# Kernel tuning notes

Hardware: AMD Instinct MI355X
Metric: run time of the kernel (lower is better)

Reference implementation:

```python
import jax, jax.numpy as jnp
import numpy as np

B, S, D, H = 4, 2048, 1024, 16
DEPTH = D // H


def setup_inputs() -> dict:
    key = jax.random.key(0)
    ks = jax.random.split(key, 12)
    q = jax.random.normal(ks[0], (B, S, D), dtype=jnp.float32)
    k = jax.random.normal(ks[1], (B, S, D), dtype=jnp.float32)
    v = jax.random.normal(ks[2], (B, S, D), dtype=jnp.float32)
    # causal mask: 1.0 where attention is disallowed (upper triangle), per `mask * -1e9`
    mask = 1.0 - jnp.tril(jnp.ones((S, S), dtype=jnp.float32))
    mask = mask[None, None, :, :]  # [1,1,S,S] broadcastable over batch/heads
    scale = 1.0 / np.sqrt(D)
    Wq = jax.random.normal(ks[3], (D, D), dtype=jnp.float32) * scale
    Wk = jax.random.normal(ks[4], (D, D), dtype=jnp.float32) * scale
    Wv = jax.random.normal(ks[5], (D, D), dtype=jnp.float32) * scale
    Wo = jax.random.normal(ks[6], (D, D), dtype=jnp.float32) * scale
    bq = jnp.zeros((D,), jnp.float32)
    bk = jnp.zeros((D,), jnp.float32)
    bv = jnp.zeros((D,), jnp.float32)
    bo = jnp.zeros((D,), jnp.float32)
    return {"query": q, "key": k, "value": v, "mask": mask,
            "Wq": Wq, "bq": bq, "Wk": Wk, "bk": bk,
            "Wv": Wv, "bv": bv, "Wo": Wo, "bo": bo}


def _split_heads(x):
    # [B, S, D] -> [B, H, S, depth]
    b, s, _ = x.shape
    return x.reshape(b, s, H, DEPTH).transpose(0, 2, 1, 3)


def reference(query, key, value, mask, Wq, bq, Wk, bk, Wv, bv, Wo, bo):
    q = _split_heads(query @ Wq + bq)   # [B,H,S,depth]
    k = _split_heads(key @ Wk + bk)
    v = _split_heads(value @ Wv + bv)
    scores = jnp.einsum('bhqd,bhkd->bhqk', q, k) / jnp.sqrt(
        jnp.asarray(DEPTH, q.dtype))
    scores = scores + mask * (-1e9)
    attn = jax.nn.softmax(scores, axis=-1)
    out = jnp.einsum('bhqk,bhkd->bhqd', attn, v)   # [B,H,S,depth]
    out = out.transpose(0, 2, 1, 3).reshape(query.shape[0], -1, H * DEPTH)
    return out @ Wo + bo
```

## Files before the change

kernel.cpp:

```cpp
#include <hip/hip_runtime.h>

#define Bsz 4
#define SEQ 2048
#define DIM 1024
#define NH 16
#define HD 64

typedef float  f32x4  __attribute__((ext_vector_type(4)));
typedef __bf16 bf16x8 __attribute__((ext_vector_type(8)));
typedef __bf16 bf16x4 __attribute__((ext_vector_type(4)));
typedef short  s16x4  __attribute__((ext_vector_type(4)));

__device__ __forceinline__ f32x4 mfma16(bf16x8 a, bf16x8 b, f32x4 c) {
    return __builtin_amdgcn_mfma_f32_16x16x32_bf16(a, b, c, 0, 0, 0);
}
__device__ __forceinline__ f32x4 mfma16k16(bf16x4 a, bf16x4 b, f32x4 c) {
#if defined(__has_builtin) && __has_builtin(__builtin_amdgcn_mfma_f32_16x16x16bf16_1k)
    return __builtin_amdgcn_mfma_f32_16x16x16bf16_1k(
        __builtin_bit_cast(s16x4, a), __builtin_bit_cast(s16x4, b), c, 0, 0, 0);
#else
    asm volatile("s_nop 2\n\tv_mfma_f32_16x16x16_bf16 %0, %1, %2, %0\n\ts_nop 7\n\ts_nop 7"
                 : "+v"(c) : "v"(a), "v"(b));
    return c;
#endif
}

#define GLD_LDS16(gsrc, ldst)                                                        \
    __builtin_amdgcn_global_load_lds(                                                \
        (const __attribute__((address_space(1))) void*)(gsrc),                       \
        (__attribute__((address_space(3))) void*)(ldst), 16, 0, 0)

__global__ __launch_bounds__(256) void wt_kernel(
    const float* __restrict__ Wq, const float* __restrict__ Wk,
    const float* __restrict__ Wv, const float* __restrict__ Wo,
    __bf16* __restrict__ wt)
{
    __shared__ float tile[64][65];
    int z = blockIdx.z;
    const float* W = (z == 0) ? Wq : (z == 1) ? Wk : (z == 2) ? Wv : Wo;
    __bf16* out = wt + (size_t)z * DIM * DIM;
    int kb = blockIdx.x * 64, nb = blockIdx.y * 64;
    int t = threadIdx.x;
    int cidx = t & 63, ridx = t >> 6;
#pragma unroll
    for (int i = 0; i < 16; i++) {
        int r = ridx + i * 4;
        tile[r][cidx] = W[(size_t)(kb + r) * DIM + nb + cidx];
    }
    __syncthreads();
#pragma unroll
    for (int i = 0; i < 16; i++) {
        int r = ridx + i * 4;
        out[(size_t)(nb + r) * DIM + kb + cidx] = (__bf16)tile[cidx][r];
    }
}

__global__ __launch_bounds__(256, 2) void gemm_proj(
    const float* __restrict__ Xq, const float* __restrict__ Xk,
    const float* __restrict__ Xv, const __bf16* __restrict__ wt,
    const float* __restrict__ bq, const float* __restrict__ bk,
    const float* __restrict__ bv,
    __bf16* __restrict__ oq, __bf16* __restrict__ ok, __bf16* __restrict__ ovT)
{
    int z = blockIdx.z;
    const float*  X    = (z == 0) ? Xq : (z == 1) ? Xk : Xv;
    const float*  bias = (z == 0) ? bq : (z == 1) ? bk : bv;
    const __bf16* Bt   = wt + (size_t)z * DIM * DIM;

    __shared__ __bf16 Abuf[128 * 32];
    __shared__ __bf16 Bbuf[128 * 32];
    __shared__ __bf16 Tt[4][64 * 72];

    int m0 = blockIdx.x * 128, n0 = blockIdx.y * 128;
    int tid = threadIdx.x, lane = tid & 63, w = tid >> 6;
    int c = lane & 15, g = lane >> 4;
    int wm = (w >> 1) * 64, wn = (w & 1) * 64;

    f32x4 acc[4][4] = {};

    int ar = tid >> 1, ah = tid & 1;
    const float* aptr = X + (size_t)(m0 + ar) * DIM + ah * 16;
    __bf16* aw = &Abuf[ar * 32 + ah * 16];

    int brow0 = (w * 2) * 16 + (lane >> 2);
    int bcol  = (lane & 3) * 8;
    const __bf16* bptr0 = Bt + (size_t)(n0 + brow0) * DIM + bcol;
    const __bf16* bptr1 = bptr0 + (size_t)16 * DIM;
    __bf16* bw0 = &Bbuf[(w * 2) * 512];
    __bf16* bw1 = &Bbuf[(w * 2 + 1) * 512];

    for (int kt = 0; kt < 32; ++kt) {
        int k0 = kt * 32;
        GLD_LDS16(bptr0 + k0, bw0);
        GLD_LDS16(bptr1 + k0, bw1);
        const float* ap = aptr + k0;
        f32x4 f0 = *(const f32x4*)(ap);
        f32x4 f1 = *(const f32x4*)(ap + 4);
        f32x4 f2 = *(const f32x4*)(ap + 8);
        f32x4 f3 = *(const f32x4*)(ap + 12);
        bf16x8 b0, b1;
#pragma unroll
        for (int j = 0; j < 4; j++) {
            b0[j]     = (__bf16)f0[j];
            b0[4 + j] = (__bf16)f1[j];
            b1[j]     = (__bf16)f2[j];
            b1[4 + j] = (__bf16)f3[j];
        }
        *(bf16x8*)(aw)     = b0;
        *(bf16x8*)(aw + 8) = b1;
        __syncthreads();

        bf16x8 af[4], bf[4];
#pragma unroll
        for (int mf = 0; mf < 4; mf++)
            af[mf] = *(bf16x8*)&Abuf[(wm + mf * 16 + c) * 32 + g * 8];
#pragma unroll
        for (int nf = 0; nf < 4; nf++)
            bf[nf] = *(bf16x8*)&Bbuf[(wn + nf * 16 + c) * 32 + g * 8];
#pragma unroll
        for (int mf = 0; mf < 4; mf++)
#pragma unroll
            for (int nf = 0; nf < 4; nf++)
                acc[mf][nf] = mfma16(af[mf], bf[nf], acc[mf][nf]);
        __syncthreads();
    }

    if (z == 2) {
        __bf16* T = Tt[w];
#pragma unroll
        for (int nf = 0; nf < 4; nf++) {
            int col = n0 + wn + nf * 16 + c;
            int d = nf * 16 + c;
            float bval = bias[col];
#pragma unroll
            for (int mf = 0; mf < 4; mf++) {
                int sl = mf * 16 + g * 4;
                bf16x4 pk;
#pragma unroll
                for (int r = 0; r < 4; r++) pk[r] = (__bf16)(acc[mf][nf][r] + bval);
                *(bf16x4*)&T[d * 72 + sl] = pk;
            }
        }
        int h = (n0 + wn) >> 6;
        int bb = m0 >> 11;
        int s_base = (m0 & (SEQ - 1)) + wm;
        int dd = lane >> 2;
        int ss = (lane & 3) * 8;
        size_t obase = ((size_t)(bb * NH + h) * HD) * SEQ;
#pragma unroll
        for (int dgrp = 0; dgrp < 4; dgrp++)
#pragma unroll
            for (int half = 0; half < 2; half++) {
                int d = dgrp * 16 + dd;
                int s = half * 32 + ss;
                bf16x8 vv = *(bf16x8*)&T[d * 72 + s];
                *(bf16x8*)&ovT[obase + (size_t)d * SEQ + s_base + s] = vv;
            }
    } else {
        __bf16* Out = (z == 0) ? oq : ok;
#pragma unroll
        for (int nf = 0; nf < 4; nf++) {
            int col = n0 + wn + nf * 16 + c;
            float bval = bias[col];
#pragma unroll
            for (int mf = 0; mf < 4; mf++) {
                int row = m0 + wm + mf * 16 + g * 4;
#pragma unroll
                for (int r = 0; r < 4; r++)
                    Out[(size_t)(row + r) * DIM + col] = (__bf16)(acc[mf][nf][r] + bval);
            }
        }
    }
}

#define QSCALE 0.180336880f

__global__ __launch_bounds__(256, 2) void fa_kernel(
    const __bf16* __restrict__ qp, const __bf16* __restrict__ kp,
    const __bf16* __restrict__ vpT, __bf16* __restrict__ op)
{
    int bz = blockIdx.x;
    int bh = bz & 63;
    int b = bh >> 4, h = bh & 15;
    int qt = 15 - (bz >> 6);
    int q0 = qt * 128;

    int tid = threadIdx.x, lane = tid & 63, w = tid >> 6;
    int c = lane & 15, g = lane >> 4;

    __shared__ __bf16 Kbuf[64 * 64];
    __shared__ __bf16 Vbuf[64 * 64];

    const int qb[2] = {q0 + w * 16, q0 + 64 + w * 16};

    bf16x8 qf[2][2];
#pragma unroll
    for (int nq = 0; nq < 2; nq++) {
        const __bf16* qbase = qp + (size_t)(b * SEQ + qb[nq] + c) * DIM + h * HD;
#pragma unroll
        for (int kc = 0; kc < 2; kc++) {
            bf16x8 raw = *(const bf16x8*)(qbase + kc * 32 + g * 8);
            bf16x8 sc;
#pragma unroll
            for (int j = 0; j < 8; j++) sc[j] = (__bf16)((float)raw[j] * QSCALE);
            qf[nq][kc] = sc;
        }
    }

    f32x4 acc[4][2] = {};
    float m_run[2] = {-1e30f, -1e30f};
    float l_run[2] = {0.f, 0.f};

    int r8 = tid >> 3, c8 = tid & 7;
    int sch = c8 ^ (r8 & 7);
    const __bf16* kbase = kp  + (size_t)(b * SEQ + r8) * DIM + h * HD + sch * 8;
    const __bf16* vbase = vpT + ((size_t)(b * NH + h) * HD + r8) * SEQ + sch * 8;
    __bf16* kdst0 = Kbuf + w * 512;
    __bf16* kdst1 = Kbuf + 2048 + w * 512;
    __bf16* vdst0 = Vbuf + w * 512;
    __bf16* vdst1 = Vbuf + 2048 + w * 512;

    int vb4[4];
#pragma unroll
    for (int mkey = 0; mkey < 4; mkey++)
        vb4[mkey] = c * 64 + (((2 * mkey + (g >> 1)) ^ (c & 7)) * 8) + (g & 1) * 4;

    int ktmax = (q0 >> 6) + 2;
    for (int kt = 0; kt < ktmax; ++kt) {
        GLD_LDS16(kbase + (size_t)kt * 64 * DIM, kdst0);
        GLD_LDS16(kbase + (size_t)(kt * 64 + 32) * DIM, kdst1);
        GLD_LDS16(vbase + kt * 64, vdst0);
        GLD_LDS16(vbase + kt * 64 + (size_t)32 * SEQ, vdst1);
        __syncthreads();

        bool need0 = (kt * 64 <= qb[0] + 15);
        int kb0 = kt * 64;

        f32x4 s[4][2] = {};
#pragma unroll
        for (int kc = 0; kc < 2; kc++) {
            bf16x8 kf[4];
#pragma unroll
            for (int mkey = 0; mkey < 4; mkey++)
                kf[mkey] = *(bf16x8*)&Kbuf[(mkey * 16 + c) * 64 + (((kc * 4 + g) ^ (c & 7)) * 8)];
#pragma unroll
            for (int mkey = 0; mkey < 4; mkey++) {
                if (need0) s[mkey][0] = mfma16(kf[mkey], qf[0][kc], s[mkey][0]);
                s[mkey][1] = mfma16(kf[mkey], qf[1][kc], s[mkey][1]);
            }
        }

        bf16x4 pf[4][2];
#pragma unroll
        for (int nq = 0; nq < 2; nq++) {
            if (nq == 0 && !need0) continue;
            int qg = qb[nq] + c;
            if (kb0 + 63 > qg) {
#pragma unroll
                for (int mkey = 0; mkey < 4; mkey++)
#pragma unroll
                    for (int r2 = 0; r2 < 4; r2++)
                        if (kb0 + mkey * 16 + g * 4 + r2 > qg) s[mkey][nq][r2] = -1e30f;
            }
            float pm0 = fmaxf(fmaxf(s[0][nq][0], s[0][nq][1]), fmaxf(s[0][nq][2], s[0][nq][3]));
            float pm1 = fmaxf(fmaxf(s[1][nq][0], s[1][nq][1]), fmaxf(s[1][nq][2], s[1][nq][3]));
            float pm2 = fmaxf(fmaxf(s[2][nq][0], s[2][nq][1]), fmaxf(s[2][nq][2], s[2][nq][3]));
            float pm3 = fmaxf(fmaxf(s[3][nq][0], s[3][nq][1]), fmaxf(s[3][nq][2], s[3][nq][3]));
            float pm = fmaxf(fmaxf(pm0, pm1), fmaxf(pm2, pm3));
            pm = fmaxf(pm, __shfl_xor(pm, 16));
            pm = fmaxf(pm, __shfl_xor(pm, 32));
            float mo = m_run[nq];
            float mn = fmaxf(mo, pm);
            m_run[nq] = mn;
            float scl = exp2f(mo - mn);
            l_run[nq] *= scl;
#pragma unroll
            for (int nf = 0; nf < 4; nf++) acc[nf][nq] *= scl;
            float rs = 0.f;
#pragma unroll
            for (int mkey = 0; mkey < 4; mkey++) {
                bf16x4 pk;
#pragma unroll
                for (int r2 = 0; r2 < 4; r2++) {
                    float p = exp2f(s[mkey][nq][r2] - mn);
                    rs += p;
                    pk[r2] = (__bf16)p;
                }
                pf[mkey][nq] = pk;
            }
            rs += __shfl_xor(rs, 16);
            rs += __shfl_xor(rs, 32);
            l_run[nq] += rs;
        }

#pragma unroll
        for (int mkey = 0; mkey < 4; mkey++) {
#pragma unroll
            for (int nf = 0; nf < 4; nf++) {
                bf16x4 vf = *(bf16x4*)&Vbuf[vb4[mkey] + nf * 1024];
                if (need0) acc[nf][0] = mfma16k16(vf, pf[mkey][0], acc[nf][0]);
                acc[nf][1] = mfma16k16(vf, pf[mkey][1], acc[nf][1]);
            }
        }
        __syncthreads();
    }

#pragma unroll
    for (int nq = 0; nq < 2; nq++) {
        float inv = 1.f / l_run[nq];
        int row = qb[nq] + c;
        __bf16* obase = op + (size_t)(b * SEQ + row) * DIM + h * HD + g * 4;
#pragma unroll
        for (int nf = 0; nf < 4; nf++) {
            bf16x4 pk;
#pragma unroll
            for (int r2 = 0; r2 < 4; r2++) pk[r2] = (__bf16)(acc[nf][nq][r2] * inv);
            *(bf16x4*)(obase + nf * 16) = pk;
        }
    }
}

__global__ __launch_bounds__(256, 2) void gemm_out(
    const __bf16* __restrict__ Ain, const __bf16* __restrict__ wt,
    const float* __restrict__ bias, float* __restrict__ Out)
{
    const __bf16* Bt = wt + (size_t)3 * DIM * DIM;

    __shared__ __bf16 Abuf[128 * 32];
    __shared__ __bf16 Bbuf[128 * 32];

    int m0 = blockIdx.x * 128, n0 = blockIdx.y * 128;
    int tid = threadIdx.x, lane = tid & 63, w = tid >> 6;
    int c = lane & 15, g = lane >> 4;
    int wm = (w >> 1) * 64, wn = (w & 1) * 64;

    f32x4 acc[4][4] = {};

    int srow = (w * 2) * 16 + (lane >> 2);
    int scol = (lane & 3) * 8;
    const __bf16* aptr0 = Ain + (size_t)(m0 + srow) * DIM + scol;
    const __bf16* aptr1 = aptr0 + (size_t)16 * DIM;
    const __bf16* bptr0 = Bt + (size_t)(n0 + srow) * DIM + scol;
    const __bf16* bptr1 = bptr0 + (size_t)16 * DIM;
    __bf16* aw0 = &Abuf[(w * 2) * 512];
    __bf16* aw1 = &Abuf[(w * 2 + 1) * 512];
    __bf16* bw0 = &Bbuf[(w * 2) * 512];
    __bf16* bw1 = &Bbuf[(w * 2 + 1) * 512];

    for (int kt = 0; kt < 32; ++kt) {
        int k0 = kt * 32;
        GLD_LDS16(aptr0 + k0, aw0);
        GLD_LDS16(aptr1 + k0, aw1);
        GLD_LDS16(bptr0 + k0, bw0);
        GLD_LDS16(bptr1 + k0, bw1);
        __syncthreads();
        bf16x8 af[4], bf[4];
#pragma unroll
        for (int mf = 0; mf < 4; mf++)
            af[mf] = *(bf16x8*)&Abuf[(wm + mf * 16 + c) * 32 + g * 8];
#pragma unroll
        for (int nf = 0; nf < 4; nf++)
            bf[nf] = *(bf16x8*)&Bbuf[(wn + nf * 16 + c) * 32 + g * 8];
#pragma unroll
        for (int mf = 0; mf < 4; mf++)
#pragma unroll
            for (int nf = 0; nf < 4; nf++)
                acc[mf][nf] = mfma16(af[mf], bf[nf], acc[mf][nf]);
        __syncthreads();
    }

#pragma unroll
    for (int nf = 0; nf < 4; nf++) {
        int col = n0 + wn + nf * 16 + c;
        float bval = bias[col];
#pragma unroll
        for (int mf = 0; mf < 4; mf++) {
            int row = m0 + wm + mf * 16 + g * 4;
#pragma unroll
            for (int r = 0; r < 4; r++)
                Out[(size_t)(row + r) * DIM + col] = acc[mf][nf][r] + bval;
        }
    }
}

extern "C" void kernel_launch(void* const* d_in, const int* in_sizes, int n_in,
                              void* d_out, int out_size, void* d_ws, size_t ws_size,
                              hipStream_t stream)
{
    const float* q  = (const float*)d_in[0];
    const float* k  = (const float*)d_in[1];
    const float* v  = (const float*)d_in[2];
    const float* Wq = (const float*)d_in[4];
    const float* bq = (const float*)d_in[5];
    const float* Wk = (const float*)d_in[6];
    const float* bk = (const float*)d_in[7];
    const float* Wv = (const float*)d_in[8];
    const float* bv = (const float*)d_in[9];
    const float* Wo = (const float*)d_in[10];
    const float* bo = (const float*)d_in[11];

    char* ws = (char*)d_ws;
    __bf16* wt  = (__bf16*)ws;
    __bf16* qp  = (__bf16*)(ws + (size_t)(8u  << 20));
    __bf16* kp  = (__bf16*)(ws + (size_t)(24u << 20));
    __bf16* vpT = (__bf16*)(ws + (size_t)(40u << 20));
    __bf16* ao  = (__bf16*)(ws + (size_t)(56u << 20));

    wt_kernel<<<dim3(16, 16, 4), 256, 0, stream>>>(Wq, Wk, Wv, Wo, wt);
    gemm_proj<<<dim3(64, 8, 3), 256, 0, stream>>>(q, k, v, wt, bq, bk, bv, qp, kp, vpT);
    fa_kernel<<<dim3(1024), 256, 0, stream>>>(qp, kp, vpT, ao);
    gemm_out<<<dim3(64, 8), 256, 0, stream>>>(ao, wt, bo, (float*)d_out);

    (void)in_sizes; (void)n_in; (void)out_size; (void)ws_size;
}
```

Before: 198.8 us.

## Double-buffer LDS tiles in projection and output GEMMs to overlap loads with MFMA

Both the QKV projection GEMM and the output GEMM now keep two LDS buffers and prefetch the next K-tile while computing on the current one, with one barrier per iteration instead of two. The projection kernel also unions its staging buffers with the transpose scratch in one shared array to keep LDS size bounded. The aim is to hide global load latency behind the MFMA work. The cost is more LDS per block for the output GEMM and more registers held across the compute for the prefetched fp32 A values, which may reduce occupancy.

```diff
diff --git a/kernel.cpp b/kernel.cpp
--- a/kernel.cpp
+++ b/kernel.cpp
@@ -67,9 +67,9 @@
     const float*  bias = (z == 0) ? bq : (z == 1) ? bk : bv;
     const __bf16* Bt   = wt + (size_t)z * DIM * DIM;
 
-    __shared__ __bf16 Abuf[128 * 32];
-    __shared__ __bf16 Bbuf[128 * 32];
-    __shared__ __bf16 Tt[4][64 * 72];
+    __shared__ __align__(16) char smem[36864];
+    __bf16* const Ab = (__bf16*)smem;
+    __bf16* const Bb = (__bf16*)(smem + 16384);
 
     int m0 = blockIdx.x * 128, n0 = blockIdx.y * 128;
     int tid = threadIdx.x, lane = tid & 63, w = tid >> 6;
@@ -80,24 +80,22 @@
 
     int ar = tid >> 1, ah = tid & 1;
     const float* aptr = X + (size_t)(m0 + ar) * DIM + ah * 16;
-    __bf16* aw = &Abuf[ar * 32 + ah * 16];
+    int awo = ar * 32 + ah * 16;
 
     int brow0 = (w * 2) * 16 + (lane >> 2);
     int bcol  = (lane & 3) * 8;
     const __bf16* bptr0 = Bt + (size_t)(n0 + brow0) * DIM + bcol;
     const __bf16* bptr1 = bptr0 + (size_t)16 * DIM;
-    __bf16* bw0 = &Bbuf[(w * 2) * 512];
-    __bf16* bw1 = &Bbuf[(w * 2 + 1) * 512];
-
-    for (int kt = 0; kt < 32; ++kt) {
-        int k0 = kt * 32;
-        GLD_LDS16(bptr0 + k0, bw0);
-        GLD_LDS16(bptr1 + k0, bw1);
-        const float* ap = aptr + k0;
-        f32x4 f0 = *(const f32x4*)(ap);
-        f32x4 f1 = *(const f32x4*)(ap + 4);
-        f32x4 f2 = *(const f32x4*)(ap + 8);
-        f32x4 f3 = *(const f32x4*)(ap + 12);
+    int bwo0 = (w * 2) * 512;
+    int bwo1 = (w * 2 + 1) * 512;
+
+    {
+        f32x4 f0 = *(const f32x4*)(aptr);
+        f32x4 f1 = *(const f32x4*)(aptr + 4);
+        f32x4 f2 = *(const f32x4*)(aptr + 8);
+        f32x4 f3 = *(const f32x4*)(aptr + 12);
+        GLD_LDS16(bptr0, Bb + bwo0);
+        GLD_LDS16(bptr1, Bb + bwo1);
         bf16x8 b0, b1;
 #pragma unroll
         for (int j = 0; j < 4; j++) {
@@ -106,27 +104,55 @@
             b1[j]     = (__bf16)f2[j];
             b1[4 + j] = (__bf16)f3[j];
         }
-        *(bf16x8*)(aw)     = b0;
-        *(bf16x8*)(aw + 8) = b1;
-        __syncthreads();
-
+        *(bf16x8*)(Ab + awo)     = b0;
+        *(bf16x8*)(Ab + awo + 8) = b1;
+    }
+    __syncthreads();
+
+    int cur = 0;
+    for (int kt = 0; kt < 32; ++kt) {
+        int nxt = kt + 1;
+        int nb = cur ^ 1;
+        f32x4 f0, f1, f2, f3;
+        if (nxt < 32) {
+            const float* ap = aptr + nxt * 32;
+            f0 = *(const f32x4*)(ap);
+            f1 = *(const f32x4*)(ap + 4);
+            f2 = *(const f32x4*)(ap + 8);
+            f3 = *(const f32x4*)(ap + 12);
+            GLD_LDS16(bptr0 + nxt * 32, Bb + nb * 4096 + bwo0);
+            GLD_LDS16(bptr1 + nxt * 32, Bb + nb * 4096 + bwo1);
+        }
         bf16x8 af[4], bf[4];
 #pragma unroll
         for (int mf = 0; mf < 4; mf++)
-            af[mf] = *(bf16x8*)&Abuf[(wm + mf * 16 + c) * 32 + g * 8];
+            af[mf] = *(bf16x8*)&Ab[cur * 4096 + (wm + mf * 16 + c) * 32 + g * 8];
 #pragma unroll
         for (int nf = 0; nf < 4; nf++)
-            bf[nf] = *(bf16x8*)&Bbuf[(wn + nf * 16 + c) * 32 + g * 8];
+            bf[nf] = *(bf16x8*)&Bb[cur * 4096 + (wn + nf * 16 + c) * 32 + g * 8];
 #pragma unroll
         for (int mf = 0; mf < 4; mf++)
 #pragma unroll
             for (int nf = 0; nf < 4; nf++)
                 acc[mf][nf] = mfma16(af[mf], bf[nf], acc[mf][nf]);
+        if (nxt < 32) {
+            bf16x8 b0, b1;
+#pragma unroll
+            for (int j = 0; j < 4; j++) {
+                b0[j]     = (__bf16)f0[j];
+                b0[4 + j] = (__bf16)f1[j];
+                b1[j]     = (__bf16)f2[j];
+                b1[4 + j] = (__bf16)f3[j];
+            }
+            *(bf16x8*)(Ab + nb * 4096 + awo)     = b0;
+            *(bf16x8*)(Ab + nb * 4096 + awo + 8) = b1;
+        }
         __syncthreads();
+        cur = nb;
     }
 
     if (z == 2) {
-        __bf16* T = Tt[w];
+        __bf16* T = (__bf16*)smem + (size_t)w * 4608;
 #pragma unroll
         for (int nf = 0; nf < 4; nf++) {
             int col = n0 + wn + nf * 16 + c;
@@ -326,8 +352,8 @@
 {
     const __bf16* Bt = wt + (size_t)3 * DIM * DIM;
 
-    __shared__ __bf16 Abuf[128 * 32];
-    __shared__ __bf16 Bbuf[128 * 32];
+    __shared__ __bf16 Ab[2][4096];
+    __shared__ __bf16 Bb[2][4096];
 
     int m0 = blockIdx.x * 128, n0 = blockIdx.y * 128;
     int tid = threadIdx.x, lane = tid & 63, w = tid >> 6;
@@ -342,31 +368,40 @@
     const __bf16* aptr1 = aptr0 + (size_t)16 * DIM;
     const __bf16* bptr0 = Bt + (size_t)(n0 + srow) * DIM + scol;
     const __bf16* bptr1 = bptr0 + (size_t)16 * DIM;
-    __bf16* aw0 = &Abuf[(w * 2) * 512];
-    __bf16* aw1 = &Abuf[(w * 2 + 1) * 512];
-    __bf16* bw0 = &Bbuf[(w * 2) * 512];
-    __bf16* bw1 = &Bbuf[(w * 2 + 1) * 512];
-
+    int so0 = (w * 2) * 512;
+    int so1 = (w * 2 + 1) * 512;
+
+    GLD_LDS16(aptr0, Ab[0] + so0);
+    GLD_LDS16(aptr1, Ab[0] + so1);
+    GLD_LDS16(bptr0, Bb[0] + so0);
+    GLD_LDS16(bptr1, Bb[0] + so1);
+    __syncthreads();
+
+    int cur = 0;
     for (int kt = 0; kt < 32; ++kt) {
-        int k0 = kt * 32;
-        GLD_LDS16(aptr0 + k0, aw0);
-        GLD_LDS16(aptr1 + k0, aw1);
-        GLD_LDS16(bptr0 + k0, bw0);
-        GLD_LDS16(bptr1 + k0, bw1);
-        __syncthreads();
+        int nxt = kt + 1;
+        int nb = cur ^ 1;
+        if (nxt < 32) {
+            int k0 = nxt * 32;
+            GLD_LDS16(aptr0 + k0, Ab[nb] + so0);
+            GLD_LDS16(aptr1 + k0, Ab[nb] + so1);
+            GLD_LDS16(bptr0 + k0, Bb[nb] + so0);
+            GLD_LDS16(bptr1 + k0, Bb[nb] + so1);
+        }
         bf16x8 af[4], bf[4];
 #pragma unroll
         for (int mf = 0; mf < 4; mf++)
-            af[mf] = *(bf16x8*)&Abuf[(wm + mf * 16 + c) * 32 + g * 8];
+            af[mf] = *(bf16x8*)&Ab[cur][(wm + mf * 16 + c) * 32 + g * 8];
 #pragma unroll
         for (int nf = 0; nf < 4; nf++)
-            bf[nf] = *(bf16x8*)&Bbuf[(wn + nf * 16 + c) * 32 + g * 8];
+            bf[nf] = *(bf16x8*)&Bb[cur][(wn + nf * 16 + c) * 32 + g * 8];
 #pragma unroll
         for (int mf = 0; mf < 4; mf++)
 #pragma unroll
             for (int nf = 0; nf < 4; nf++)
                 acc[mf][nf] = mfma16(af[mf], bf[nf], acc[mf][nf]);
         __syncthreads();
+        cur = nb;
     }
 
 #pragma unroll
```

New measurement: 201.1 us. No clear change (+1.1%).
